# Optimization experiments

Hardware: AMD Instinct MI355X
Metric: run time of the kernel (lower is better)

The kernel has to match this reference:

```python
import jax, jax.numpy as jnp
import numpy as np


def _bs_matrix(n):
    # Kronecker product of n copies of the 2x2 beam-splitter unitary.
    bs = (1.0 / np.sqrt(2.0)) * np.array([[1 + 0j, 0 + 1j], [0 + 1j, 1 + 0j]], dtype=np.complex128)
    M = np.array([[1.0 + 0j]], dtype=np.complex128)
    for _ in range(n):
        M = np.kron(M, bs)
    return jnp.asarray(M, dtype=jnp.complex64)  # [2^n, 2^n]


def _phase_shifts(phi0, phi1, n):
    # Equivalent to phase_shifts_to_tensor_product_space_v2:
    # phi[i] = sum_q (phi1[q] if bit_{n-1-q}(i) else phi0[q]); returns exp(i*phi).
    N = 2 ** n
    bits = (jnp.arange(N)[:, None] >> (n - 1 - jnp.arange(n))[None, :]) & 1  # [N, n]
    bits = bits.astype(phi0.dtype)
    phi = jnp.sum(bits * phi1 + (1.0 - bits) * phi0, axis=-1)  # [N]
    return jax.lax.complex(jnp.cos(phi), jnp.sin(phi))


def setup_inputs() -> dict:
    n = 12
    N = 2 ** n
    B = 2048
    key = jax.random.key(0)
    kx, ka, kb, kt, kp = jax.random.split(key, 5)
    TWO_PI = 2.0 * np.pi
    return {
        "x": jax.random.normal(kx, (B, 2, N), dtype=jnp.float32),
        "alphas": jax.random.uniform(ka, (n,), dtype=jnp.float32, minval=0.0, maxval=TWO_PI),
        "betas": jax.random.uniform(kb, (n,), dtype=jnp.float32, minval=0.0, maxval=TWO_PI),
        "thetas": jax.random.uniform(kt, (n,), dtype=jnp.float32, minval=0.0, maxval=TWO_PI),
        "phis": jax.random.uniform(kp, (n,), dtype=jnp.float32, minval=0.0, maxval=TWO_PI),
    }


def reference(x, alphas, betas, thetas, phis):
    n = alphas.shape[0]
    bs = _bs_matrix(n)  # [N, N] complex
    input_shifts = _phase_shifts(alphas, betas, n)                       # [N]
    theta_shifts = _phase_shifts(thetas, jnp.zeros_like(thetas), n)      # [N]
    phi_shifts = _phase_shifts(phis, jnp.zeros_like(phis), n)            # [N]

    z = jax.lax.complex(x[:, 0, :], x[:, 1, :])  # [B, N]
    out = (input_shifts * z) @ bs
    out = (theta_shifts * out) @ bs
    out = phi_shifts * out
    return jnp.stack([jnp.real(out), jnp.imag(out)], axis=1)  # [B, 2, N]
```

## Files before the change

### kernel.cpp

```cpp
#include <hip/hip_runtime.h>
#include <math.h>

#define NQ 12
#define NN 4096

typedef float f2 __attribute__((ext_vector_type(2)));
typedef float f4 __attribute__((ext_vector_type(4)));

__device__ __forceinline__ float2 cmulh(float2 a, float2 b) {
    return make_float2(a.x * b.x - a.y * b.y, a.x * b.y + a.y * b.x);
}

__device__ __forceinline__ f2 rfl2(f2 a) {
    f2 r;
    r.x = __int_as_float(__builtin_amdgcn_readfirstlane(__float_as_int(a.x)));
    r.y = __int_as_float(__builtin_amdgcn_readfirstlane(__float_as_int(a.y)));
    return r;
}

__device__ __forceinline__ void cmac_pk(f2& acc, f2 m, f2 b) {
    asm("v_pk_fma_f32 %0, %1, %2, %0 op_sel:[0,0,0] op_sel_hi:[0,1,1]\n\t"
        "v_pk_fma_f32 %0, %1, %2, %0 op_sel:[1,1,0] op_sel_hi:[1,0,1] neg_lo:[1,0,0]"
        : "+v"(acc) : "s"(m), "v"(b));
}
__device__ __forceinline__ void cmul_pk(f2& r, f2 m, f2 b) {
    asm("v_pk_mul_f32 %0, %1, %2 op_sel:[0,0] op_sel_hi:[0,1]\n\t"
        "v_pk_fma_f32 %0, %1, %2, %0 op_sel:[1,1,0] op_sel_hi:[1,0,1] neg_lo:[1,0,0]"
        : "=&v"(r) : "s"(m), "v"(b));
}

template<int D>
__device__ __forceinline__ void stagepk8(f2 (&v)[8], f2 m00, f2 m01, f2 m10, f2 m11) {
    #pragma unroll
    for (int s = 0; s < 8; ++s) {
        if (s & D) continue;
        f2 va = v[s], vb = v[s | D];
        f2 r0, r1;
        cmul_pk(r0, m00, va); cmac_pk(r0, m01, vb);
        cmul_pk(r1, m10, va); cmac_pk(r1, m11, vb);
        v[s] = r0; v[s | D] = r1;
    }
}

__global__ __launch_bounds__(512, 8) void sq_layer(const float* __restrict__ x,
                                                   float* __restrict__ out,
                                                   const float* __restrict__ alphas,
                                                   const float* __restrict__ betas,
                                                   const float* __restrict__ thetas,
                                                   const float* __restrict__ phis) {
    __shared__ f2 lds[4608];
    __shared__ __align__(16) f2 Msh[48];
    const int T = threadIdx.x;
    const size_t row0 = (size_t)blockIdx.x * 2;

    const float* px = x + row0 * (2 * NN) + (T << 3);
    float4 ra0 = *reinterpret_cast<const float4*>(px);
    float4 rb0 = *reinterpret_cast<const float4*>(px + 4);
    float4 ia0 = *reinterpret_cast<const float4*>(px + NN);
    float4 ib0 = *reinterpret_cast<const float4*>(px + NN + 4);
    float4 ra1 = *reinterpret_cast<const float4*>(px + 2 * NN);
    float4 rb1 = *reinterpret_cast<const float4*>(px + 2 * NN + 4);
    float4 ia1 = *reinterpret_cast<const float4*>(px + 3 * NN);
    float4 ib1 = *reinterpret_cast<const float4*>(px + 3 * NN + 4);

    if (T < NQ) {
        int p = T, q = NQ - 1 - p;
        float av = alphas[q], bv = betas[q], tv = thetas[q], fv = phis[q];
        float sa = __sinf(av), ca = __cosf(av);
        float sb = __sinf(bv), cb = __cosf(bv);
        float st = __sinf(tv), ct = __cosf(tv);
        float sf = __sinf(fv), cf = __cosf(fv);
        float2 A  = make_float2(ca, sa);
        float2 Bb = make_float2(cb, sb);
        float2 F  = make_float2(cf, sf);
        float2 Tm  = make_float2(0.5f * (ct - 1.0f), 0.5f * st);
        float2 Tp  = make_float2(0.5f * (ct + 1.0f), 0.5f * st);
        float2 iTp = make_float2(-Tp.y, Tp.x);
        float2 m00 = cmulh(cmulh(F, Tm), A);
        float2 m01 = cmulh(cmulh(F, iTp), Bb);
        float2 m10 = cmulh(iTp, A);
        float2 m11 = cmulh(make_float2(-Tm.x, -Tm.y), Bb);
        Msh[p * 4 + 0] = f2{m00.x, m00.y};
        Msh[p * 4 + 1] = f2{m01.x, m01.y};
        Msh[p * 4 + 2] = f2{m10.x, m10.y};
        Msh[p * 4 + 3] = f2{m11.x, m11.y};
    }
    __syncthreads();

    f2 M[48];
    #pragma unroll
    for (int k = 0; k < 24; ++k) {
        f4 two = *reinterpret_cast<const f4*>(&Msh[k * 2]);
        M[k * 2 + 0] = rfl2(f2{two.x, two.y});
        M[k * 2 + 1] = rfl2(f2{two.z, two.w});
    }

    #pragma unroll
    for (int r = 0; r < 2; ++r) {
        f2 v[8];
        if (r == 0) {
            v[0] = f2{ra0.x, ia0.x}; v[1] = f2{ra0.y, ia0.y};
            v[2] = f2{ra0.z, ia0.z}; v[3] = f2{ra0.w, ia0.w};
            v[4] = f2{rb0.x, ib0.x}; v[5] = f2{rb0.y, ib0.y};
            v[6] = f2{rb0.z, ib0.z}; v[7] = f2{rb0.w, ib0.w};
        } else {
            v[0] = f2{ra1.x, ia1.x}; v[1] = f2{ra1.y, ia1.y};
            v[2] = f2{ra1.z, ia1.z}; v[3] = f2{ra1.w, ia1.w};
            v[4] = f2{rb1.x, ib1.x}; v[5] = f2{rb1.y, ib1.y};
            v[6] = f2{rb1.z, ib1.z}; v[7] = f2{rb1.w, ib1.w};
        }

        stagepk8<1>(v, M[0],  M[1],  M[2],  M[3]);
        stagepk8<2>(v, M[4],  M[5],  M[6],  M[7]);
        stagepk8<4>(v, M[8],  M[9],  M[10], M[11]);

        {
            f2* wp = lds + 9 * T;
            #pragma unroll
            for (int s = 0; s < 8; ++s) wp[s] = v[s];
        }
        {
            const f2* rp = lds + 72 * (T >> 3) + (T & 7);
            #pragma unroll
            for (int s = 0; s < 8; ++s) v[s] = rp[9 * s];
        }

        stagepk8<1>(v, M[12], M[13], M[14], M[15]);
        stagepk8<2>(v, M[16], M[17], M[18], M[19]);
        stagepk8<4>(v, M[20], M[21], M[22], M[23]);

        {
            f2* wp = lds + 72 * (T >> 3) + (T & 7);
            #pragma unroll
            for (int s = 0; s < 8; ++s) wp[9 * s] = v[s];
        }
        {
            const f2* rp = lds + 576 * (T >> 6) + (T & 63) + ((T & 63) >> 3);
            #pragma unroll
            for (int s = 0; s < 8; ++s) v[s] = rp[72 * s];
        }

        stagepk8<1>(v, M[24], M[25], M[26], M[27]);
        stagepk8<2>(v, M[28], M[29], M[30], M[31]);
        stagepk8<4>(v, M[32], M[33], M[34], M[35]);

        {
            f2* wp = lds + 576 * (T >> 6) + (T & 63) + ((T & 63) >> 3);
            #pragma unroll
            for (int s = 0; s < 8; ++s) wp[72 * s] = v[s];
        }
        __syncthreads();
        {
            const f2* rp = lds + T + (T >> 3);
            #pragma unroll
            for (int s = 0; s < 8; ++s) v[s] = rp[576 * s];
        }
        if (r == 0) __syncthreads();

        stagepk8<1>(v, M[36], M[37], M[38], M[39]);
        stagepk8<2>(v, M[40], M[41], M[42], M[43]);
        stagepk8<4>(v, M[44], M[45], M[46], M[47]);

        {
            float* po = out + (row0 + r) * (2 * NN);
            #pragma unroll
            for (int s = 0; s < 8; ++s) {
                int i = (s << 9) | T;
                __builtin_nontemporal_store(v[s].x, po + i);
                __builtin_nontemporal_store(v[s].y, po + NN + i);
            }
        }
    }
}

extern "C" void kernel_launch(void* const* d_in, const int* in_sizes, int n_in,
                              void* d_out, int out_size, void* d_ws, size_t ws_size,
                              hipStream_t stream) {
    const float* x      = (const float*)d_in[0];
    const float* alphas = (const float*)d_in[1];
    const float* betas  = (const float*)d_in[2];
    const float* thetas = (const float*)d_in[3];
    const float* phis   = (const float*)d_in[4];
    float* out = (float*)d_out;

    const int B = in_sizes[0] / (2 * NN);

    hipLaunchKernelGGL(sq_layer, dim3(B / 2), dim3(512), 0, stream,
                       x, out, alphas, betas, thetas, phis);
}
```

Baseline: 28.82 us.

## Interleave the two rows' butterfly stages to overlap LDS transposes with compute

Replaces the sequential two-row loop with a hand-interleaved schedule. The wave-local LDS transposes of one row now sit between the butterfly stages of the other row, so LDS latency can hide behind independent packed-FMA work. The two block-wide syncs are rearranged so each row keeps its cross-wave transpose. Both rows' state is now live at once, which raises register pressure and may limit occupancy.

```diff
diff --git a/kernel.cpp b/kernel.cpp
--- a/kernel.cpp
+++ b/kernel.cpp
@@ -39,6 +39,51 @@
         cmul_pk(r0, m00, va); cmac_pk(r0, m01, vb);
         cmul_pk(r1, m10, va); cmac_pk(r1, m11, vb);
         v[s] = r0; v[s | D] = r1;
+    }
+}
+
+__device__ __forceinline__ void phase3(f2 (&v)[8], const f2* Mp) {
+    stagepk8<1>(v, Mp[0], Mp[1], Mp[2],  Mp[3]);
+    stagepk8<2>(v, Mp[4], Mp[5], Mp[6],  Mp[7]);
+    stagepk8<4>(v, Mp[8], Mp[9], Mp[10], Mp[11]);
+}
+
+__device__ __forceinline__ void t1w(f2* lds, int T, f2 (&v)[8]) {
+    f2* wp = lds + 9 * T;
+    #pragma unroll
+    for (int s = 0; s < 8; ++s) wp[s] = v[s];
+}
+__device__ __forceinline__ void t1r(f2* lds, int T, f2 (&v)[8]) {
+    const f2* rp = lds + 72 * (T >> 3) + (T & 7);
+    #pragma unroll
+    for (int s = 0; s < 8; ++s) v[s] = rp[9 * s];
+}
+__device__ __forceinline__ void t2w(f2* lds, int T, f2 (&v)[8]) {
+    f2* wp = lds + 72 * (T >> 3) + (T & 7);
+    #pragma unroll
+    for (int s = 0; s < 8; ++s) wp[9 * s] = v[s];
+}
+__device__ __forceinline__ void t2r(f2* lds, int T, f2 (&v)[8]) {
+    const f2* rp = lds + 576 * (T >> 6) + (T & 63) + ((T & 63) >> 3);
+    #pragma unroll
+    for (int s = 0; s < 8; ++s) v[s] = rp[72 * s];
+}
+__device__ __forceinline__ void t3w(f2* lds, int T, f2 (&v)[8]) {
+    f2* wp = lds + 576 * (T >> 6) + (T & 63) + ((T & 63) >> 3);
+    #pragma unroll
+    for (int s = 0; s < 8; ++s) wp[72 * s] = v[s];
+}
+__device__ __forceinline__ void dread(f2* lds, int T, f2 (&v)[8]) {
+    const f2* rp = lds + T + (T >> 3);
+    #pragma unroll
+    for (int s = 0; s < 8; ++s) v[s] = rp[576 * s];
+}
+__device__ __forceinline__ void storeD(float* po, int T, f2 (&v)[8]) {
+    #pragma unroll
+    for (int s = 0; s < 8; ++s) {
+        int i = (s << 9) | T;
+        __builtin_nontemporal_store(v[s].x, po + i);
+        __builtin_nontemporal_store(v[s].y, po + NN + i);
     }
 }
 
@@ -95,82 +140,42 @@
         M[k * 2 + 1] = rfl2(f2{two.z, two.w});
     }
 
-    #pragma unroll
-    for (int r = 0; r < 2; ++r) {
-        f2 v[8];
-        if (r == 0) {
-            v[0] = f2{ra0.x, ia0.x}; v[1] = f2{ra0.y, ia0.y};
-            v[2] = f2{ra0.z, ia0.z}; v[3] = f2{ra0.w, ia0.w};
-            v[4] = f2{rb0.x, ib0.x}; v[5] = f2{rb0.y, ib0.y};
-            v[6] = f2{rb0.z, ib0.z}; v[7] = f2{rb0.w, ib0.w};
-        } else {
-            v[0] = f2{ra1.x, ia1.x}; v[1] = f2{ra1.y, ia1.y};
-            v[2] = f2{ra1.z, ia1.z}; v[3] = f2{ra1.w, ia1.w};
-            v[4] = f2{rb1.x, ib1.x}; v[5] = f2{rb1.y, ib1.y};
-            v[6] = f2{rb1.z, ib1.z}; v[7] = f2{rb1.w, ib1.w};
-        }
+    f2 v0[8], v1[8];
+    v0[0] = f2{ra0.x, ia0.x}; v0[1] = f2{ra0.y, ia0.y};
+    v0[2] = f2{ra0.z, ia0.z}; v0[3] = f2{ra0.w, ia0.w};
+    v0[4] = f2{rb0.x, ib0.x}; v0[5] = f2{rb0.y, ib0.y};
+    v0[6] = f2{rb0.z, ib0.z}; v0[7] = f2{rb0.w, ib0.w};
 
-        stagepk8<1>(v, M[0],  M[1],  M[2],  M[3]);
-        stagepk8<2>(v, M[4],  M[5],  M[6],  M[7]);
-        stagepk8<4>(v, M[8],  M[9],  M[10], M[11]);
+    phase3(v0, M + 0);
+    t1w(lds, T, v0); t1r(lds, T, v0);
 
-        {
-            f2* wp = lds + 9 * T;
-            #pragma unroll
-            for (int s = 0; s < 8; ++s) wp[s] = v[s];
-        }
-        {
-            const f2* rp = lds + 72 * (T >> 3) + (T & 7);
-            #pragma unroll
-            for (int s = 0; s < 8; ++s) v[s] = rp[9 * s];
-        }
+    v1[0] = f2{ra1.x, ia1.x}; v1[1] = f2{ra1.y, ia1.y};
+    v1[2] = f2{ra1.z, ia1.z}; v1[3] = f2{ra1.w, ia1.w};
+    v1[4] = f2{rb1.x, ib1.x}; v1[5] = f2{rb1.y, ib1.y};
+    v1[6] = f2{rb1.z, ib1.z}; v1[7] = f2{rb1.w, ib1.w};
+    phase3(v1, M + 0);
 
-        stagepk8<1>(v, M[12], M[13], M[14], M[15]);
-        stagepk8<2>(v, M[16], M[17], M[18], M[19]);
-        stagepk8<4>(v, M[20], M[21], M[22], M[23]);
+    phase3(v0, M + 12);
+    t2w(lds, T, v0); t2r(lds, T, v0);
+    t1w(lds, T, v1); t1r(lds, T, v1);
 
-        {
-            f2* wp = lds + 72 * (T >> 3) + (T & 7);
-            #pragma unroll
-            for (int s = 0; s < 8; ++s) wp[9 * s] = v[s];
-        }
-        {
-            const f2* rp = lds + 576 * (T >> 6) + (T & 63) + ((T & 63) >> 3);
-            #pragma unroll
-            for (int s = 0; s < 8; ++s) v[s] = rp[72 * s];
-        }
+    phase3(v0, M + 24);
+    phase3(v1, M + 12);
 
-        stagepk8<1>(v, M[24], M[25], M[26], M[27]);
-        stagepk8<2>(v, M[28], M[29], M[30], M[31]);
-        stagepk8<4>(v, M[32], M[33], M[34], M[35]);
+    t3w(lds, T, v0);
+    __syncthreads();
+    dread(lds, T, v0);
+    phase3(v0, M + 36);
+    storeD(out + row0 * (2 * NN), T, v0);
+    __syncthreads();
 
-        {
-            f2* wp = lds + 576 * (T >> 6) + (T & 63) + ((T & 63) >> 3);
-            #pragma unroll
-            for (int s = 0; s < 8; ++s) wp[72 * s] = v[s];
-        }
-        __syncthreads();
-        {
-            const f2* rp = lds + T + (T >> 3);
-            #pragma unroll
-            for (int s = 0; s < 8; ++s) v[s] = rp[576 * s];
-        }
-        if (r == 0) __syncthreads();
-
-        stagepk8<1>(v, M[36], M[37], M[38], M[39]);
-        stagepk8<2>(v, M[40], M[41], M[42], M[43]);
-        stagepk8<4>(v, M[44], M[45], M[46], M[47]);
-
-        {
-            float* po = out + (row0 + r) * (2 * NN);
-            #pragma unroll
-            for (int s = 0; s < 8; ++s) {
-                int i = (s << 9) | T;
-                __builtin_nontemporal_store(v[s].x, po + i);
-                __builtin_nontemporal_store(v[s].y, po + NN + i);
-            }
-        }
-    }
+    t2w(lds, T, v1); t2r(lds, T, v1);
+    phase3(v1, M + 24);
+    t3w(lds, T, v1);
+    __syncthreads();
+    dread(lds, T, v1);
+    phase3(v1, M + 36);
+    storeD(out + (row0 + 1) * (2 * NN), T, v1);
 }
 
 extern "C" void kernel_launch(void* const* d_in, const int* in_sizes, int n_in,
```

After: 39.38 us. 1.37x slower.
